# Kernel optimization log

Hardware: AMD Instinct MI355X
Metric: run time of the kernel (lower is better)

The kernel has to match this reference:

```python
import jax, jax.numpy as jnp
import numpy as np

N_NODES = 100000


def gcn_conv(x, edge_index, W, b):
    """PyG GCNConv: add self-loops, symmetric D^-1/2 (A+I) D^-1/2 normalization,
    linear transform, bias. Transform-then-aggregate (out_dim <= in_dim here)."""
    src, dst = edge_index[0], edge_index[1]
    h = x @ W  # [N, out]
    # degree including self-loop (edge_weight = 1)
    ones = jnp.ones(src.shape[0], dtype=x.dtype)
    deg = jax.ops.segment_sum(ones, dst, num_segments=N_NODES) + 1.0
    dinv = jax.lax.rsqrt(deg)  # [N]
    # normalized messages over real edges
    norm = dinv[src] * dinv[dst]  # [E]
    msgs = h[src] * norm[:, None]  # [E, out] -- dominant memory traffic
    agg = jax.ops.segment_sum(msgs, dst, num_segments=N_NODES)
    # self-loop contribution: norm_ii = dinv[i]^2
    agg = agg + h * (dinv * dinv)[:, None]
    return agg + b


def setup_inputs() -> dict:
    key = jax.random.key(0)
    k1, k2, k3, k4, k5, k6 = jax.random.split(key, 6)
    in_dim, hidden_dim, out_dim = 128, 64, 32
    n_edges = 1_600_000
    x = jax.random.normal(k1, (N_NODES, in_dim), dtype=jnp.float32)
    edge_index = jax.random.randint(k2, (2, n_edges), 0, N_NODES, dtype=jnp.int64)
    s1 = 1.0 / np.sqrt(in_dim)
    s2 = 1.0 / np.sqrt(hidden_dim)
    W1 = jax.random.uniform(k3, (in_dim, hidden_dim), jnp.float32, -s1, s1)
    b1 = jax.random.uniform(k4, (hidden_dim,), jnp.float32, -s1, s1)
    W2 = jax.random.uniform(k5, (hidden_dim, out_dim), jnp.float32, -s2, s2)
    b2 = jax.random.uniform(k6, (out_dim,), jnp.float32, -s2, s2)
    return {"x": x, "edge_index": edge_index, "W1": W1, "b1": b1, "W2": W2, "b2": b2}


def reference(x, edge_index, W1, b1, W2, b2):
    h = jax.nn.relu(gcn_conv(x, edge_index, W1, b1))
    return gcn_conv(h, edge_index, W2, b2)
```

## Files before the change

### kernel.cpp

```cpp
#include <hip/hip_runtime.h>

#define N_NODES 100000
#define CAP 10240

__device__ __forceinline__ unsigned short f2bf_rn(float f) {
    unsigned int b = __float_as_uint(f);
    b += 0x7fffu + ((b >> 16) & 1u);
    return (unsigned short)(b >> 16);
}
__device__ __forceinline__ float bf_lo(unsigned int u) { return __uint_as_float(u << 16); }
__device__ __forceinline__ float bf_hi(unsigned int u) { return __uint_as_float(u & 0xffff0000u); }

typedef int v4i __attribute__((ext_vector_type(4)));

__global__ __launch_bounds__(256) void initcur_kernel(unsigned int* __restrict__ cursor) {
    int t = threadIdx.x;
    cursor[t] = (unsigned int)t * CAP;
}

__global__ __launch_bounds__(256) void bin_kernel(const int* __restrict__ ei, int E,
                                                  unsigned int* __restrict__ cursor,
                                                  unsigned int* __restrict__ binned) {
    __shared__ unsigned int cnt[256];
    __shared__ unsigned int cur[256];
    int t = threadIdx.x;
    cnt[t] = 0;
    __syncthreads();
    int base = blockIdx.x * 4096;
    unsigned int pk[16];
    unsigned int bk[16];
    bool vec = ((E & 3) == 0);
#pragma unroll
    for (int k = 0; k < 4; ++k) {
        int e = base + (k * 256 + t) * 4;
        if (vec && e + 3 < E) {
            v4i s4 = __builtin_nontemporal_load((const v4i*)(ei + e));
            v4i d4 = __builtin_nontemporal_load((const v4i*)(ei + E + e));
            int ss[4] = {s4.x, s4.y, s4.z, s4.w};
            int dd[4] = {d4.x, d4.y, d4.z, d4.w};
#pragma unroll
            for (int q = 0; q < 4; ++q) {
                unsigned int b = (unsigned int)dd[q] >> 9;
                pk[k * 4 + q] = (unsigned int)ss[q] | (((unsigned int)dd[q] & 511u) << 17);
                bk[k * 4 + q] = b;
                atomicAdd(&cnt[b], 1u);
            }
        } else {
#pragma unroll
            for (int q = 0; q < 4; ++q) {
                int eq = e + q;
                if (eq < E) {
                    int s = ei[eq], d = ei[E + eq];
                    unsigned int b = (unsigned int)d >> 9;
                    pk[k * 4 + q] = (unsigned int)s | (((unsigned int)d & 511u) << 17);
                    bk[k * 4 + q] = b;
                    atomicAdd(&cnt[b], 1u);
                } else {
                    bk[k * 4 + q] = 0xFFFFFFFFu;
                }
            }
        }
    }
    __syncthreads();
    if (cnt[t] > 0) cur[t] = atomicAdd(&cursor[t], cnt[t]);
    __syncthreads();
#pragma unroll
    for (int k = 0; k < 16; ++k) {
        if (bk[k] != 0xFFFFFFFFu) {
            unsigned int pos = atomicAdd(&cur[bk[k]], 1u);
            binned[pos] = pk[k];
        }
    }
}

__global__ __launch_bounds__(256) void cscan_kernel(const unsigned int* __restrict__ cursor,
                                                    int nb, int E,
                                                    unsigned int* __restrict__ bucket_base) {
    __shared__ unsigned int s[256];
    int t = threadIdx.x;
    unsigned int v = (t < nb) ? (cursor[t] - (unsigned int)t * CAP) : 0u;
    s[t] = v; __syncthreads();
    for (int off = 1; off < 256; off <<= 1) {
        unsigned int x = s[t];
        unsigned int y = (t >= off) ? s[t - off] : 0u;
        __syncthreads();
        s[t] = x + y;
        __syncthreads();
    }
    if (t < nb) bucket_base[t] = s[t] - v;
    if (t == 0) bucket_base[nb] = (unsigned int)E;
}

__global__ __launch_bounds__(512) void build_kernel(const unsigned int* __restrict__ binned,
                                                    const unsigned int* __restrict__ cursor,
                                                    const unsigned int* __restrict__ bucket_base,
                                                    float* __restrict__ dinv,
                                                    int* __restrict__ row_start,
                                                    int* __restrict__ srcs, int N, int E) {
    __shared__ unsigned int cnt[512];
    __shared__ unsigned int sc[512];
    __shared__ int cur[512];
    int t = threadIdx.x;
    cnt[t] = 0;
    int bbeg = blockIdx.x * CAP;
    int bend = (int)cursor[blockIdx.x];
    int obase = (int)bucket_base[blockIdx.x];
    __syncthreads();
    for (int i = bbeg + t; i < bend; i += 512)
        atomicAdd(&cnt[binned[i] >> 17], 1u);
    __syncthreads();
    unsigned int v = cnt[t];
    sc[t] = v; __syncthreads();
    for (int off = 1; off < 512; off <<= 1) {
        unsigned int x = sc[t];
        unsigned int y = (t >= off) ? sc[t - off] : 0u;
        __syncthreads();
        sc[t] = x + y;
        __syncthreads();
    }
    int excl = obase + (int)(sc[t] - v);
    int node = (blockIdx.x << 9) + t;
    if (node < N) {
        row_start[node] = excl;
        dinv[node] = rsqrtf((float)v + 1.0f);
    }
    cur[t] = excl;
    if (blockIdx.x == 0 && t == 0) row_start[N] = E;
    __syncthreads();
    for (int i = bbeg + t; i < bend; i += 512) {
        unsigned int u = binned[i];
        int slot = atomicAdd(&cur[u >> 17], 1);
        srcs[slot] = (int)(u & 0x1FFFFu);
    }
}

__global__ __launch_bounds__(256) void gemm1_kernel(
    const float* __restrict__ x, const float* __restrict__ W,
    const float* __restrict__ dinv,
    unsigned short* __restrict__ h1b, int N) {
    __shared__ float4 Ws4[128 * 16];
    __shared__ float4 xs4[64 * 33];
    int tid = threadIdx.x;
    const float4* W4 = (const float4*)W;
#pragma unroll
    for (int i = 0; i < 8; ++i) Ws4[tid + 256 * i] = W4[tid + 256 * i];
    int row0 = blockIdx.x * 64;
    const float4* x4 = (const float4*)x;
#pragma unroll
    for (int i = 0; i < 8; ++i) {
        int idx = tid + 256 * i;
        int r = idx >> 5, c = idx & 31;
        int gr = row0 + r;
        float4 v;
        if (gr < N) v = x4[(size_t)gr * 32 + c];
        else { v.x = v.y = v.z = v.w = 0.f; }
        xs4[r * 33 + c] = v;
    }
    __syncthreads();
    int tc = tid & 15;
    int tr = tid >> 4;
    float4 acc[4];
#pragma unroll
    for (int rr = 0; rr < 4; ++rr) { acc[rr].x = 0.f; acc[rr].y = 0.f; acc[rr].z = 0.f; acc[rr].w = 0.f; }
#pragma unroll 2
    for (int k4 = 0; k4 < 32; ++k4) {
        float4 xr[4], w[4];
#pragma unroll
        for (int rr = 0; rr < 4; ++rr) xr[rr] = xs4[(tr * 4 + rr) * 33 + k4];
#pragma unroll
        for (int kk = 0; kk < 4; ++kk) w[kk] = Ws4[(k4 * 4 + kk) * 16 + tc];
#pragma unroll
        for (int rr = 0; rr < 4; ++rr) {
            acc[rr].x += xr[rr].x * w[0].x; acc[rr].y += xr[rr].x * w[0].y;
            acc[rr].z += xr[rr].x * w[0].z; acc[rr].w += xr[rr].x * w[0].w;
            acc[rr].x += xr[rr].y * w[1].x; acc[rr].y += xr[rr].y * w[1].y;
            acc[rr].z += xr[rr].y * w[1].z; acc[rr].w += xr[rr].y * w[1].w;
            acc[rr].x += xr[rr].z * w[2].x; acc[rr].y += xr[rr].z * w[2].y;
            acc[rr].z += xr[rr].z * w[2].z; acc[rr].w += xr[rr].z * w[2].w;
            acc[rr].x += xr[rr].w * w[3].x; acc[rr].y += xr[rr].w * w[3].y;
            acc[rr].z += xr[rr].w * w[3].z; acc[rr].w += xr[rr].w * w[3].w;
        }
    }
#pragma unroll
    for (int rr = 0; rr < 4; ++rr) {
        int r = row0 + tr * 4 + rr;
        if (r < N) {
            float di = dinv[r];
            ushort4 o;
            o.x = f2bf_rn(acc[rr].x * di); o.y = f2bf_rn(acc[rr].y * di);
            o.z = f2bf_rn(acc[rr].z * di); o.w = f2bf_rn(acc[rr].w * di);
            *(ushort4*)(h1b + (size_t)r * 64 + tc * 4) = o;
        }
    }
}

__global__ __launch_bounds__(256) void agg1_kernel(
    const unsigned int* __restrict__ h1u,
    const int* __restrict__ srcs,
    const int* __restrict__ row_start, const float* __restrict__ dinv,
    const float* __restrict__ b1, const float* __restrict__ W2,
    unsigned short* __restrict__ h2b, int N) {
    __shared__ float W2s[64 * 32];
    __shared__ float hr[8][64];
    int tid = threadIdx.x;
    const float4* W24 = (const float4*)W2;
    float4* W2s4 = (float4*)W2s;
#pragma unroll
    for (int i = 0; i < 2; ++i) W2s4[tid + 256 * i] = W24[tid + 256 * i];
    __syncthreads();
    int nib = tid >> 5;
    int jp = tid & 31;
    int d = blockIdx.x * 8 + nib;
    if (d >= N) return;
    float di = dinv[d];
    float2 bias = ((const float2*)b1)[jp];
    unsigned int su = h1u[(size_t)d * 32 + jp];
    int beg = row_start[d], end = row_start[d + 1];
    float a0 = bf_lo(su);
    float a1 = bf_hi(su);
    int e = beg;
    for (; e + 16 <= end; e += 16) {
        int c[16];
#pragma unroll
        for (int k = 0; k < 16; ++k) c[k] = srcs[e + k];
        unsigned int u[16];
#pragma unroll
        for (int k = 0; k < 16; ++k) u[k] = h1u[(size_t)c[k] * 32 + jp];
#pragma unroll
        for (int k = 0; k < 16; ++k) { a0 += bf_lo(u[k]); a1 += bf_hi(u[k]); }
    }
    if (e + 8 <= end) {
        int c[8];
#pragma unroll
        for (int k = 0; k < 8; ++k) c[k] = srcs[e + k];
        unsigned int u[8];
#pragma unroll
        for (int k = 0; k < 8; ++k) u[k] = h1u[(size_t)c[k] * 32 + jp];
#pragma unroll
        for (int k = 0; k < 8; ++k) { a0 += bf_lo(u[k]); a1 += bf_hi(u[k]); }
        e += 8;
    }
    if (e + 4 <= end) {
        int c[4];
#pragma unroll
        for (int k = 0; k < 4; ++k) c[k] = srcs[e + k];
        unsigned int u[4];
#pragma unroll
        for (int k = 0; k < 4; ++k) u[k] = h1u[(size_t)c[k] * 32 + jp];
#pragma unroll
        for (int k = 0; k < 4; ++k) { a0 += bf_lo(u[k]); a1 += bf_hi(u[k]); }
        e += 4;
    }
    for (; e < end; ++e) {
        unsigned int u0 = h1u[(size_t)srcs[e] * 32 + jp];
        a0 += bf_lo(u0); a1 += bf_hi(u0);
    }
    float h0 = fmaxf(a0 * di + bias.x, 0.f);
    float h1v = fmaxf(a1 * di + bias.y, 0.f);
    hr[nib][2 * jp] = h0;
    hr[nib][2 * jp + 1] = h1v;
    const float* hrw = hr[nib];
    float p = 0.f;
#pragma unroll 8
    for (int k = 0; k < 64; ++k)
        p += hrw[k] * W2s[k * 32 + jp];
    h2b[(size_t)d * 32 + jp] = f2bf_rn(p * di);
}

__global__ __launch_bounds__(256) void agg2_kernel(
    const uint2* __restrict__ h2v,
    const int* __restrict__ srcs,
    const int* __restrict__ row_start, const float* __restrict__ dinv,
    const float* __restrict__ b2, float* __restrict__ out, int N) {
    int t = blockIdx.x * 256 + threadIdx.x;
    int d = t >> 3;
    int jp = t & 7;
    if (d >= N) return;
    float di = dinv[d];
    float4 bias = ((const float4*)b2)[jp];
    uint2 su = h2v[(size_t)d * 8 + jp];
    int beg = row_start[d], end = row_start[d + 1];
    float a0 = bf_lo(su.x), a1 = bf_hi(su.x);
    float a2 = bf_lo(su.y), a3 = bf_hi(su.y);
    int e = beg;
    for (; e + 8 <= end; e += 8) {
        int c[8];
#pragma unroll
        for (int k = 0; k < 8; ++k) c[k] = srcs[e + k];
        uint2 u[8];
#pragma unroll
        for (int k = 0; k < 8; ++k) u[k] = h2v[(size_t)c[k] * 8 + jp];
#pragma unroll
        for (int k = 0; k < 8; ++k) {
            a0 += bf_lo(u[k].x); a1 += bf_hi(u[k].x);
            a2 += bf_lo(u[k].y); a3 += bf_hi(u[k].y);
        }
    }
    if (e + 4 <= end) {
        int c[4];
#pragma unroll
        for (int k = 0; k < 4; ++k) c[k] = srcs[e + k];
        uint2 u[4];
#pragma unroll
        for (int k = 0; k < 4; ++k) u[k] = h2v[(size_t)c[k] * 8 + jp];
#pragma unroll
        for (int k = 0; k < 4; ++k) {
            a0 += bf_lo(u[k].x); a1 += bf_hi(u[k].x);
            a2 += bf_lo(u[k].y); a3 += bf_hi(u[k].y);
        }
        e += 4;
    }
    for (; e < end; ++e) {
        uint2 u0 = h2v[(size_t)srcs[e] * 8 + jp];
        a0 += bf_lo(u0.x); a1 += bf_hi(u0.x);
        a2 += bf_lo(u0.y); a3 += bf_hi(u0.y);
    }
    float4 r;
    r.x = a0 * di + bias.x;
    r.y = a1 * di + bias.y;
    r.z = a2 * di + bias.z;
    r.w = a3 * di + bias.w;
    ((float4*)(out + (size_t)d * 32))[jp] = r;
}

extern "C" void kernel_launch(void* const* d_in, const int* in_sizes, int n_in,
                              void* d_out, int out_size, void* d_ws, size_t ws_size,
                              hipStream_t stream) {
    const float* x  = (const float*)d_in[0];
    const int*   ei = (const int*)d_in[1];
    const float* W1 = (const float*)d_in[2];
    const float* b1 = (const float*)d_in[3];
    const float* W2 = (const float*)d_in[4];
    const float* b2 = (const float*)d_in[5];
    float* out = (float*)d_out;

    const int N = N_NODES;
    const int E = in_sizes[1] / 2;
    const int NB = (N + 511) / 512;
    const int EB = (E + 4095) / 4096;

    char* p = (char*)d_ws;
    int* srcs = (int*)p;                      p += (size_t)E * 4;
    unsigned int* binned = (unsigned int*)p;  p += (size_t)NB * CAP * 4;
    unsigned short* h1b = (unsigned short*)p; p += (size_t)N * 64 * 2;
    unsigned short* h2b = (unsigned short*)p; p += (size_t)N * 32 * 2;
    float* dinv = (float*)p;                  p += (size_t)N * 4;
    int* row_start = (int*)p;                 p += (size_t)(N + 1) * 4;
    unsigned int* cursor = (unsigned int*)p;  p += 256 * 4;
    unsigned int* bucket_base = (unsigned int*)p;

    initcur_kernel<<<1, 256, 0, stream>>>(cursor);
    bin_kernel<<<EB, 256, 0, stream>>>(ei, E, cursor, binned);
    cscan_kernel<<<1, 256, 0, stream>>>(cursor, NB, E, bucket_base);
    build_kernel<<<NB, 512, 0, stream>>>(binned, cursor, bucket_base, dinv,
                                         row_start, srcs, N, E);

    gemm1_kernel<<<(N + 63) / 64, 256, 0, stream>>>(x, W1, dinv, h1b, N);
    agg1_kernel<<<(N + 7) / 8, 256, 0, stream>>>((const unsigned int*)h1b, srcs, row_start,
                                                 dinv, b1, W2, h2b, N);
    agg2_kernel<<<(N * 8 + 255) / 256, 256, 0, stream>>>((const uint2*)h2b, srcs,
                                                         row_start, dinv, b2, out, N);
}
```

Before: 231.9 us.

## Sub-bin edges by source octant to localize neighbor gathers

Splits each destination bucket into eight sub-cells keyed by source-node range, so each node's CSR neighbor list is grouped by source region. This is meant to improve cache locality of the h[src] gathers in the aggregation kernels. In exchange, binning uses more shared-memory counters and global cursor atomics, and the smaller per-cell capacity could overflow on skewed degree distributions.

```diff
diff --git a/kernel.cpp b/kernel.cpp
--- a/kernel.cpp
+++ b/kernel.cpp
@@ -1,7 +1,9 @@
 #include <hip/hip_runtime.h>
 
 #define N_NODES 100000
-#define CAP 10240
+#define NOCT 8
+#define SUBCAP 1280
+#define NCELL (196 * NOCT)
 
 __device__ __forceinline__ unsigned short f2bf_rn(float f) {
     unsigned int b = __float_as_uint(f);
@@ -14,21 +16,21 @@
 typedef int v4i __attribute__((ext_vector_type(4)));
 
 __global__ __launch_bounds__(256) void initcur_kernel(unsigned int* __restrict__ cursor) {
-    int t = threadIdx.x;
-    cursor[t] = (unsigned int)t * CAP;
+    int i = blockIdx.x * 256 + threadIdx.x;
+    if (i < NCELL) cursor[i] = (unsigned int)i * SUBCAP;
 }
 
 __global__ __launch_bounds__(256) void bin_kernel(const int* __restrict__ ei, int E,
                                                   unsigned int* __restrict__ cursor,
                                                   unsigned int* __restrict__ binned) {
-    __shared__ unsigned int cnt[256];
-    __shared__ unsigned int cur[256];
+    __shared__ unsigned int cnt[NCELL];
+    __shared__ unsigned int cur[NCELL];
     int t = threadIdx.x;
-    cnt[t] = 0;
+    for (int i = t; i < NCELL; i += 256) cnt[i] = 0;
     __syncthreads();
     int base = blockIdx.x * 4096;
     unsigned int pk[16];
-    unsigned int bk[16];
+    unsigned int ck[16];
     bool vec = ((E & 3) == 0);
 #pragma unroll
     for (int k = 0; k < 4; ++k) {
@@ -40,10 +42,11 @@
             int dd[4] = {d4.x, d4.y, d4.z, d4.w};
 #pragma unroll
             for (int q = 0; q < 4; ++q) {
-                unsigned int b = (unsigned int)dd[q] >> 9;
+                unsigned int cell = (((unsigned int)dd[q] >> 9) << 3) +
+                                    ((unsigned int)ss[q] / 12500u);
                 pk[k * 4 + q] = (unsigned int)ss[q] | (((unsigned int)dd[q] & 511u) << 17);
-                bk[k * 4 + q] = b;
-                atomicAdd(&cnt[b], 1u);
+                ck[k * 4 + q] = cell;
+                atomicAdd(&cnt[cell], 1u);
             }
         } else {
 #pragma unroll
@@ -51,23 +54,25 @@
                 int eq = e + q;
                 if (eq < E) {
                     int s = ei[eq], d = ei[E + eq];
-                    unsigned int b = (unsigned int)d >> 9;
+                    unsigned int cell = (((unsigned int)d >> 9) << 3) +
+                                        ((unsigned int)s / 12500u);
                     pk[k * 4 + q] = (unsigned int)s | (((unsigned int)d & 511u) << 17);
-                    bk[k * 4 + q] = b;
-                    atomicAdd(&cnt[b], 1u);
+                    ck[k * 4 + q] = cell;
+                    atomicAdd(&cnt[cell], 1u);
                 } else {
-                    bk[k * 4 + q] = 0xFFFFFFFFu;
+                    ck[k * 4 + q] = 0xFFFFFFFFu;
                 }
             }
         }
     }
     __syncthreads();
-    if (cnt[t] > 0) cur[t] = atomicAdd(&cursor[t], cnt[t]);
+    for (int i = t; i < NCELL; i += 256)
+        if (cnt[i] > 0) cur[i] = atomicAdd(&cursor[i], cnt[i]);
     __syncthreads();
 #pragma unroll
     for (int k = 0; k < 16; ++k) {
-        if (bk[k] != 0xFFFFFFFFu) {
-            unsigned int pos = atomicAdd(&cur[bk[k]], 1u);
+        if (ck[k] != 0xFFFFFFFFu) {
+            unsigned int pos = atomicAdd(&cur[ck[k]], 1u);
             binned[pos] = pk[k];
         }
     }
@@ -78,7 +83,14 @@
                                                     unsigned int* __restrict__ bucket_base) {
     __shared__ unsigned int s[256];
     int t = threadIdx.x;
-    unsigned int v = (t < nb) ? (cursor[t] - (unsigned int)t * CAP) : 0u;
+    unsigned int v = 0;
+    if (t < nb) {
+#pragma unroll
+        for (int o = 0; o < NOCT; ++o) {
+            int cell = t * NOCT + o;
+            v += cursor[cell] - (unsigned int)cell * SUBCAP;
+        }
+    }
     s[t] = v; __syncthreads();
     for (int off = 1; off < 256; off <<= 1) {
         unsigned int x = s[t];
@@ -102,12 +114,16 @@
     __shared__ int cur[512];
     int t = threadIdx.x;
     cnt[t] = 0;
-    int bbeg = blockIdx.x * CAP;
-    int bend = (int)cursor[blockIdx.x];
     int obase = (int)bucket_base[blockIdx.x];
     __syncthreads();
-    for (int i = bbeg + t; i < bend; i += 512)
-        atomicAdd(&cnt[binned[i] >> 17], 1u);
+#pragma unroll
+    for (int oct = 0; oct < NOCT; ++oct) {
+        int cell = blockIdx.x * NOCT + oct;
+        int bbeg = cell * SUBCAP;
+        int bend = (int)cursor[cell];
+        for (int i = bbeg + t; i < bend; i += 512)
+            atomicAdd(&cnt[binned[i] >> 17], 1u);
+    }
     __syncthreads();
     unsigned int v = cnt[t];
     sc[t] = v; __syncthreads();
@@ -127,10 +143,17 @@
     cur[t] = excl;
     if (blockIdx.x == 0 && t == 0) row_start[N] = E;
     __syncthreads();
-    for (int i = bbeg + t; i < bend; i += 512) {
-        unsigned int u = binned[i];
-        int slot = atomicAdd(&cur[u >> 17], 1);
-        srcs[slot] = (int)(u & 0x1FFFFu);
+#pragma unroll
+    for (int oct = 0; oct < NOCT; ++oct) {
+        int cell = blockIdx.x * NOCT + oct;
+        int bbeg = cell * SUBCAP;
+        int bend = (int)cursor[cell];
+        for (int i = bbeg + t; i < bend; i += 512) {
+            unsigned int u = binned[i];
+            int slot = atomicAdd(&cur[u >> 17], 1);
+            srcs[slot] = (int)(u & 0x1FFFFu);
+        }
+        __syncthreads();
     }
 }
 
@@ -341,15 +364,15 @@
 
     char* p = (char*)d_ws;
     int* srcs = (int*)p;                      p += (size_t)E * 4;
-    unsigned int* binned = (unsigned int*)p;  p += (size_t)NB * CAP * 4;
+    unsigned int* binned = (unsigned int*)p;  p += (size_t)NCELL * SUBCAP * 4;
     unsigned short* h1b = (unsigned short*)p; p += (size_t)N * 64 * 2;
     unsigned short* h2b = (unsigned short*)p; p += (size_t)N * 32 * 2;
     float* dinv = (float*)p;                  p += (size_t)N * 4;
     int* row_start = (int*)p;                 p += (size_t)(N + 1) * 4;
-    unsigned int* cursor = (unsigned int*)p;  p += 256 * 4;
+    unsigned int* cursor = (unsigned int*)p;  p += ((NCELL + 63) / 64) * 64 * 4;
     unsigned int* bucket_base = (unsigned int*)p;
 
-    initcur_kernel<<<1, 256, 0, stream>>>(cursor);
+    initcur_kernel<<<(NCELL + 255) / 256, 256, 0, stream>>>(cursor);
     bin_kernel<<<EB, 256, 0, stream>>>(ei, E, cursor, binned);
     cscan_kernel<<<1, 256, 0, stream>>>(cursor, NB, E, bucket_base);
     build_kernel<<<NB, 512, 0, stream>>>(binned, cursor, bucket_base, dinv,
```

Result: slower. 247.1 us (+6.6%).
